# Performance work log

Hardware: AMD Instinct MI355X
Metric: run time of the kernel (lower is better)

Reference implementation:

```python
import jax, jax.numpy as jnp
import numpy as np

N = 100000
E = 1600000
IN_C, HID, OUT_C = 128, 64, 64


def gcn_conv(x, src, dst, W, b, n):
    # PyG GCNConv: h = D^{-1/2} (A + I) D^{-1/2} (x @ W) + b
    h = x @ W  # [N, F_out]
    # degrees from edges + self-loops (edge weight 1)
    deg = jax.ops.segment_sum(jnp.ones_like(dst, dtype=h.dtype), dst, num_segments=n)
    deg = deg + 1.0  # self-loops
    dinv = jnp.where(deg > 0, jax.lax.rsqrt(deg), 0.0)
    norm = dinv[src] * dinv[dst]  # [E]
    out = jax.ops.segment_sum(h[src] * norm[:, None], dst, num_segments=n)
    out = out + h * (dinv * dinv)[:, None]  # self-loop messages
    return out + b


def setup_inputs() -> dict:
    key = jax.random.key(0)
    ks = jax.random.split(key, 8)
    x = jax.random.normal(ks[0], (N, IN_C), dtype=jnp.float32)
    edge_index = jax.random.randint(ks[1], (2, E), 0, N, dtype=jnp.int64)
    def glorot(k, fan_in, fan_out):
        s = jnp.sqrt(6.0 / (fan_in + fan_out))
        return jax.random.uniform(k, (fan_in, fan_out), jnp.float32, -s, s)
    return {
        "x": x,
        "edge_index": edge_index,
        "W1": glorot(ks[2], IN_C, HID),
        "b1": jnp.zeros((HID,), jnp.float32),
        "W_mu": glorot(ks[3], HID, OUT_C),
        "b_mu": jnp.zeros((OUT_C,), jnp.float32),
        "W_ls": glorot(ks[4], HID, OUT_C),
        "b_ls": jnp.zeros((OUT_C,), jnp.float32),
    }


def reference(x, edge_index, W1, b1, W_mu, b_mu, W_ls, b_ls):
    src, dst = edge_index[0], edge_index[1]
    h = jax.nn.relu(gcn_conv(x, src, dst, W1, b1, N))
    mu = gcn_conv(h, src, dst, W_mu, b_mu, N)
    logstd = gcn_conv(h, src, dst, W_ls, b_ls, N)
    return mu, logstd
```

## Files before the change

### kernel.cpp

```cpp
#include <hip/hip_runtime.h>


using uint = unsigned int;

static constexpr int FEAT = 64;
static constexpr int BN = 256;
static constexpr int SORT_BLOCKS = 256;
static constexpr int NB_MAX = 512;

typedef __attribute__((ext_vector_type(8))) short bf16x8;
typedef __attribute__((ext_vector_type(4))) float f32x4;

static __device__ __forceinline__ ushort f2bf(float f) {
    uint u = __float_as_uint(f);
    u += 0x7FFFu + ((u >> 16) & 1u);
    return (ushort)(u >> 16);
}
static __device__ __forceinline__ float bf2f(ushort b) {
    return __uint_as_float(((uint)b) << 16);
}


__global__ __launch_bounds__(256) void hist_kernel(const int* __restrict__ dst,
                                                   int* __restrict__ hist, int E, int nb) {
    __shared__ int h[NB_MAX];
    for (int i = threadIdx.x; i < nb; i += 256) h[i] = 0;
    __syncthreads();
    int chunk = (E + SORT_BLOCKS - 1) / SORT_BLOCKS;
    int beg = blockIdx.x * chunk;
    int end = min(beg + chunk, E);
    for (int e = beg + (int)threadIdx.x; e < end; e += 256)
        atomicAdd(&h[dst[e] >> 8], 1);
    __syncthreads();
    for (int i = threadIdx.x; i < nb; i += 256) hist[blockIdx.x * nb + i] = h[i];
}

__global__ __launch_bounds__(256) void colscan_kernel(int* __restrict__ hist,
                                                      int* __restrict__ btot, int nb) {
    __shared__ int s[256];
    int b = blockIdx.x;
    int t = threadIdx.x;
    int v = hist[t * nb + b];
    s[t] = v; __syncthreads();
    for (int off = 1; off < 256; off <<= 1) {
        int u = (t >= off) ? s[t - off] : 0;
        __syncthreads();
        s[t] += u;
        __syncthreads();
    }
    hist[t * nb + b] = s[t] - v;
    if (t == 255) btot[b] = s[255];
}

__global__ __launch_bounds__(256) void bbase_kernel(const int* __restrict__ btot,
                                                    int* __restrict__ bbase, int nb,
                                                    int* __restrict__ rowptr, int n, int E) {
    __shared__ int s[256];
    int t = threadIdx.x;
    int i0 = 2 * t, i1 = 2 * t + 1;
    int v0 = (i0 < nb) ? btot[i0] : 0;
    int v1 = (i1 < nb) ? btot[i1] : 0;
    s[t] = v0 + v1; __syncthreads();
    for (int off = 1; off < 256; off <<= 1) {
        int u = (t >= off) ? s[t - off] : 0;
        __syncthreads();
        s[t] += u;
        __syncthreads();
    }
    int excl = s[t] - (v0 + v1);
    if (i0 < nb) bbase[i0] = excl;
    if (i1 < nb) bbase[i1] = excl + v0;
    if (i0 == nb) bbase[nb] = excl;
    else if (i1 == nb) bbase[nb] = excl + v0;
    if (t == 0) rowptr[n] = E;
}

__global__ __launch_bounds__(256) void sort_scatter_kernel(const int* __restrict__ src,
                                                           const int* __restrict__ dst,
                                                           const int* __restrict__ hist,
                                                           const int* __restrict__ bbase,
                                                           uint* __restrict__ bpk, int E, int nb) {
    __shared__ int cur[NB_MAX];
    int k = blockIdx.x;
    for (int i = threadIdx.x; i < nb; i += 256) cur[i] = bbase[i] + hist[k * nb + i];
    __syncthreads();
    int chunk = (E + SORT_BLOCKS - 1) / SORT_BLOCKS;
    int beg = k * chunk;
    int end = min(beg + chunk, E);
    for (int e = beg + (int)threadIdx.x; e < end; e += 256) {
        int s = src[e], d = dst[e];
        int pos = atomicAdd(&cur[d >> 8], 1);
        bpk[pos] = (uint)s | ((uint)(d & 255) << 17);
    }
}

__global__ __launch_bounds__(256) void place_kernel(const uint* __restrict__ bpk,
                                                    const int* __restrict__ bbase,
                                                    int* __restrict__ rowptr,
                                                    float* __restrict__ dinv,
                                                    int* __restrict__ ssrc, int n) {
    __shared__ int cnt[BN];
    __shared__ int s[256];
    int b = blockIdx.x;
    int base = b * BN;
    int beg = bbase[b], end = bbase[b + 1];
    cnt[threadIdx.x] = 0;
    __syncthreads();
    for (int p = beg + (int)threadIdx.x; p < end; p += 256)
        atomicAdd(&cnt[bpk[p] >> 17], 1);
    __syncthreads();
    int c = cnt[threadIdx.x];
    s[threadIdx.x] = c; __syncthreads();
    for (int off = 1; off < 256; off <<= 1) {
        int u = (threadIdx.x >= off) ? s[threadIdx.x - off] : 0;
        __syncthreads();
        s[threadIdx.x] += u;
        __syncthreads();
    }
    int excl = beg + s[threadIdx.x] - c;
    __syncthreads();
    cnt[threadIdx.x] = excl;
    int node = base + threadIdx.x;
    if (node < n) {
        rowptr[node] = excl;
        dinv[node] = rsqrtf((float)c + 1.0f);
    }
    __syncthreads();
    for (int p = beg + (int)threadIdx.x; p < end; p += 256) {
        uint e = bpk[p];
        int pos = atomicAdd(&cnt[e >> 17], 1);
        ssrc[pos] = (int)(e & 0x1FFFFu);
    }
}

__global__ __launch_bounds__(256) void prep_w_kernel(const float* __restrict__ W1,
                                                     const float* __restrict__ Wmu,
                                                     const float* __restrict__ Wls,
                                                     ushort* __restrict__ w1t,
                                                     ushort* __restrict__ wmt,
                                                     ushort* __restrict__ wlt) {
    int t = blockIdx.x * 256 + threadIdx.x;
    for (int idx = t; idx < 64 * 128; idx += 2048) {
        int nn = idx >> 7, kk = idx & 127;
        w1t[idx] = f2bf(W1[kk * 64 + nn]);
    }
    for (int idx = t; idx < 64 * 64; idx += 2048) {
        int nn = idx >> 6, kk = idx & 63;
        wmt[idx] = f2bf(Wmu[kk * 64 + nn]);
        wlt[idx] = f2bf(Wls[kk * 64 + nn]);
    }
}

__global__ __launch_bounds__(256) void gemm1_kernel(const float* __restrict__ X,
                                                    const ushort* __restrict__ Wt,
                                                    const float* __restrict__ dinv,
                                                    ushort* __restrict__ T1, int n) {
    int lane = threadIdx.x & 63;
    int w = threadIdx.x >> 6;
    int rowbase = blockIdx.x * 64 + w * 16;
    int nl = lane & 15;
    int kg = lane >> 4;
    int arow = min(rowbase + nl, n - 1);
    const float* xr = X + (size_t)arow * 128 + kg * 8;
    f32x4 acc0 = {0.f, 0.f, 0.f, 0.f};
    f32x4 acc1 = acc0, acc2 = acc0, acc3 = acc0;
#pragma unroll
    for (int ks = 0; ks < 4; ++ks) {
        int k0 = ks * 32;
        float4 xa = *(const float4*)(xr + k0);
        float4 xb = *(const float4*)(xr + k0 + 4);
        bf16x8 a;
        a[0] = (short)f2bf(xa.x); a[1] = (short)f2bf(xa.y);
        a[2] = (short)f2bf(xa.z); a[3] = (short)f2bf(xa.w);
        a[4] = (short)f2bf(xb.x); a[5] = (short)f2bf(xb.y);
        a[6] = (short)f2bf(xb.z); a[7] = (short)f2bf(xb.w);
        const ushort* wb = Wt + (size_t)nl * 128 + k0 + kg * 8;
        bf16x8 b0 = *(const bf16x8*)(wb);
        bf16x8 b1 = *(const bf16x8*)(wb + 16 * 128);
        bf16x8 b2 = *(const bf16x8*)(wb + 32 * 128);
        bf16x8 b3 = *(const bf16x8*)(wb + 48 * 128);
        acc0 = __builtin_amdgcn_mfma_f32_16x16x32_bf16(a, b0, acc0, 0, 0, 0);
        acc1 = __builtin_amdgcn_mfma_f32_16x16x32_bf16(a, b1, acc1, 0, 0, 0);
        acc2 = __builtin_amdgcn_mfma_f32_16x16x32_bf16(a, b2, acc2, 0, 0, 0);
        acc3 = __builtin_amdgcn_mfma_f32_16x16x32_bf16(a, b3, acc3, 0, 0, 0);
    }
#pragma unroll
    for (int r = 0; r < 4; ++r) {
        int row = rowbase + kg * 4 + r;
        if (row < n) {
            float di = dinv[row];
            ushort* out = T1 + (size_t)row * FEAT + nl;
            out[0]  = f2bf(acc0[r] * di);
            out[16] = f2bf(acc1[r] * di);
            out[32] = f2bf(acc2[r] * di);
            out[48] = f2bf(acc3[r] * di);
        }
    }
}

template<int MODE>
__global__ __launch_bounds__(256) void agg_kernel(const ushort* __restrict__ T,
                                                  const int* __restrict__ rowptr,
                                                  const int* __restrict__ ssrc,
                                                  const float* __restrict__ dinv,
                                                  const float* __restrict__ bias,
                                                  ushort* __restrict__ Tout, int n) {
    int node = blockIdx.x * 4 + (threadIdx.x >> 6);
    if (node >= n) return;
    int f = threadIdx.x & 63;
    int beg = rowptr[node], end = rowptr[node + 1];
    float di = dinv[node];
    float acc = bf2f(T[(size_t)node * FEAT + f]);
    int p = beg;
    int ahead = (beg + 3) & ~3;
    for (int lim = min(ahead, end); p < lim; ++p)
        acc += bf2f(T[(size_t)ssrc[p] * FEAT + f]);
    for (; p + 8 <= end; p += 8) {
        int4 a = *(const int4*)(ssrc + p);
        int4 b = *(const int4*)(ssrc + p + 4);
        float v0 = bf2f(T[(size_t)a.x * FEAT + f]);
        float v1 = bf2f(T[(size_t)a.y * FEAT + f]);
        float v2 = bf2f(T[(size_t)a.z * FEAT + f]);
        float v3 = bf2f(T[(size_t)a.w * FEAT + f]);
        float v4 = bf2f(T[(size_t)b.x * FEAT + f]);
        float v5 = bf2f(T[(size_t)b.y * FEAT + f]);
        float v6 = bf2f(T[(size_t)b.z * FEAT + f]);
        float v7 = bf2f(T[(size_t)b.w * FEAT + f]);
        acc += ((v0 + v1) + (v2 + v3)) + ((v4 + v5) + (v6 + v7));
    }
    if (p + 4 <= end) {
        int4 a = *(const int4*)(ssrc + p);
        float v0 = bf2f(T[(size_t)a.x * FEAT + f]);
        float v1 = bf2f(T[(size_t)a.y * FEAT + f]);
        float v2 = bf2f(T[(size_t)a.z * FEAT + f]);
        float v3 = bf2f(T[(size_t)a.w * FEAT + f]);
        acc += (v0 + v1) + (v2 + v3);
        p += 4;
    }
    for (; p < end; ++p) acc += bf2f(T[(size_t)ssrc[p] * FEAT + f]);
    if (MODE == 0) {
        float h = fmaf(di, acc, bias[f]);
        h = fmaxf(h, 0.0f);
        Tout[(size_t)node * FEAT + f] = f2bf(h * di);
    } else {
        Tout[(size_t)node * FEAT + f] = f2bf(di * acc);
    }
}

__global__ __launch_bounds__(256) void gemm_dual_kernel(const ushort* __restrict__ H,
                                                        const ushort* __restrict__ Wmt,
                                                        const float* __restrict__ bmu,
                                                        const ushort* __restrict__ Wlt,
                                                        const float* __restrict__ bls,
                                                        float* __restrict__ mu,
                                                        float* __restrict__ ls, int n) {
    int lane = threadIdx.x & 63;
    int w = threadIdx.x >> 6;
    int rowbase = blockIdx.x * 64 + w * 16;
    int nl = lane & 15;
    int kg = lane >> 4;
    int arow = min(rowbase + nl, n - 1);
    const ushort* hr = H + (size_t)arow * 64 + kg * 8;
    f32x4 am0 = {0.f, 0.f, 0.f, 0.f};
    f32x4 am1 = am0, am2 = am0, am3 = am0;
    f32x4 al0 = am0, al1 = am0, al2 = am0, al3 = am0;
#pragma unroll
    for (int ks = 0; ks < 2; ++ks) {
        int k0 = ks * 32;
        bf16x8 a = *(const bf16x8*)(hr + k0);
        const ushort* wm = Wmt + (size_t)nl * 64 + k0 + kg * 8;
        const ushort* wl = Wlt + (size_t)nl * 64 + k0 + kg * 8;
        bf16x8 m0 = *(const bf16x8*)(wm);
        bf16x8 m1 = *(const bf16x8*)(wm + 16 * 64);
        bf16x8 m2 = *(const bf16x8*)(wm + 32 * 64);
        bf16x8 m3 = *(const bf16x8*)(wm + 48 * 64);
        bf16x8 l0 = *(const bf16x8*)(wl);
        bf16x8 l1 = *(const bf16x8*)(wl + 16 * 64);
        bf16x8 l2 = *(const bf16x8*)(wl + 32 * 64);
        bf16x8 l3 = *(const bf16x8*)(wl + 48 * 64);
        am0 = __builtin_amdgcn_mfma_f32_16x16x32_bf16(a, m0, am0, 0, 0, 0);
        am1 = __builtin_amdgcn_mfma_f32_16x16x32_bf16(a, m1, am1, 0, 0, 0);
        am2 = __builtin_amdgcn_mfma_f32_16x16x32_bf16(a, m2, am2, 0, 0, 0);
        am3 = __builtin_amdgcn_mfma_f32_16x16x32_bf16(a, m3, am3, 0, 0, 0);
        al0 = __builtin_amdgcn_mfma_f32_16x16x32_bf16(a, l0, al0, 0, 0, 0);
        al1 = __builtin_amdgcn_mfma_f32_16x16x32_bf16(a, l1, al1, 0, 0, 0);
        al2 = __builtin_amdgcn_mfma_f32_16x16x32_bf16(a, l2, al2, 0, 0, 0);
        al3 = __builtin_amdgcn_mfma_f32_16x16x32_bf16(a, l3, al3, 0, 0, 0);
    }
    float bm0 = bmu[nl], bm1 = bmu[16 + nl], bm2 = bmu[32 + nl], bm3 = bmu[48 + nl];
    float bl0 = bls[nl], bl1 = bls[16 + nl], bl2 = bls[32 + nl], bl3 = bls[48 + nl];
#pragma unroll
    for (int r = 0; r < 4; ++r) {
        int row = rowbase + kg * 4 + r;
        if (row < n) {
            float* om = mu + (size_t)row * 64 + nl;
            float* ol = ls + (size_t)row * 64 + nl;
            om[0]  = am0[r] + bm0; om[16] = am1[r] + bm1;
            om[32] = am2[r] + bm2; om[48] = am3[r] + bm3;
            ol[0]  = al0[r] + bl0; ol[16] = al1[r] + bl1;
            ol[32] = al2[r] + bl2; ol[48] = al3[r] + bl3;
        }
    }
}

extern "C" void kernel_launch(void* const* d_in, const int* in_sizes, int n_in,
                              void* d_out, int out_size, void* d_ws, size_t ws_size,
                              hipStream_t stream) {
    const float* x   = (const float*)d_in[0];
    const int*   ei  = (const int*)d_in[1];
    const float* W1  = (const float*)d_in[2];
    const float* b1  = (const float*)d_in[3];
    const float* Wmu = (const float*)d_in[4];
    const float* bmu = (const float*)d_in[5];
    const float* Wls = (const float*)d_in[6];
    const float* bls = (const float*)d_in[7];

    const int N = in_sizes[0] / 128;
    const int E = in_sizes[1] / 2;
    const int* src = ei;
    const int* dst = ei + E;

    const int nb = (N + BN - 1) / BN;

    float*  dinv   = (float*)d_ws;
    int*    rowptr = (int*)(dinv + N);
    int*    hist   = rowptr + ((N + 1 + 63) & ~63);
    int*    btot   = hist + SORT_BLOCKS * nb;
    int*    bbase  = btot + ((nb + 63) & ~63);
    int*    ssrc   = bbase + ((nb + 1 + 63) & ~63);
    uint*   bpk    = (uint*)(ssrc + E);
    ushort* T1     = (ushort*)(bpk + E);
    ushort* T2     = T1 + (size_t)N * FEAT;
    ushort* w1t    = T2 + (size_t)N * FEAT;
    ushort* wmt    = w1t + 64 * 128;
    ushort* wlt    = wmt + 64 * 64;

    float* mu_out = (float*)d_out;
    float* ls_out = mu_out + (size_t)N * FEAT;

    const int TB = 256;
    int grid_n4 = (N + 3) / 4;
    int grid_g  = (N + 63) / 64;

    prep_w_kernel<<<8, TB, 0, stream>>>(W1, Wmu, Wls, w1t, wmt, wlt);

    hist_kernel<<<SORT_BLOCKS, TB, 0, stream>>>(dst, hist, E, nb);
    colscan_kernel<<<nb, TB, 0, stream>>>(hist, btot, nb);
    bbase_kernel<<<1, TB, 0, stream>>>(btot, bbase, nb, rowptr, N, E);
    sort_scatter_kernel<<<SORT_BLOCKS, TB, 0, stream>>>(src, dst, hist, bbase, bpk, E, nb);
    place_kernel<<<nb, TB, 0, stream>>>(bpk, bbase, rowptr, dinv, ssrc, N);

    gemm1_kernel<<<grid_g, TB, 0, stream>>>(x, w1t, dinv, T1, N);

    agg_kernel<0><<<grid_n4, TB, 0, stream>>>(T1, rowptr, ssrc, dinv, b1, T2, N);

    agg_kernel<1><<<grid_n4, TB, 0, stream>>>(T2, rowptr, ssrc, dinv, nullptr, T1, N);

    gemm_dual_kernel<<<grid_g, TB, 0, stream>>>(T1, wmt, bmu, wlt, bls, mu_out, ls_out, N);
}
```

Before: 217.1 us.

## Fuse per-node CSR placement into aggregation via shared-memory bucket sort

Drops the separate place kernel that built rowptr and a global sorted source array. Each aggregation block now re-sorts its 256-node bucket of packed edges into shared memory (capacity 5120 edges) and aggregates straight from there. Degrees come from global atomics in the histogram pass plus a small dinv kernel. This removes a global scatter pass and the rowptr/ssrc traffic, but the per-bucket sort is repeated in both aggregation passes. It also adds per-edge global atomics and a hard bucket-size cap that could overflow on skewed graphs.

```diff
diff --git a/kernel.cpp b/kernel.cpp
--- a/kernel.cpp
+++ b/kernel.cpp
@@ -7,6 +7,8 @@
 static constexpr int BN = 256;
 static constexpr int SORT_BLOCKS = 256;
 static constexpr int NB_MAX = 512;
+static constexpr int AGG_TPB = 1024;
+static constexpr int ECAP = 5120;
 
 typedef __attribute__((ext_vector_type(8))) short bf16x8;
 typedef __attribute__((ext_vector_type(4))) float f32x4;
@@ -22,17 +24,27 @@
 
 
 __global__ __launch_bounds__(256) void hist_kernel(const int* __restrict__ dst,
-                                                   int* __restrict__ hist, int E, int nb) {
+                                                   int* __restrict__ hist,
+                                                   int* __restrict__ deg, int E, int nb) {
     __shared__ int h[NB_MAX];
     for (int i = threadIdx.x; i < nb; i += 256) h[i] = 0;
     __syncthreads();
     int chunk = (E + SORT_BLOCKS - 1) / SORT_BLOCKS;
     int beg = blockIdx.x * chunk;
     int end = min(beg + chunk, E);
-    for (int e = beg + (int)threadIdx.x; e < end; e += 256)
-        atomicAdd(&h[dst[e] >> 8], 1);
+    for (int e = beg + (int)threadIdx.x; e < end; e += 256) {
+        int d = dst[e];
+        atomicAdd(&h[d >> 8], 1);
+        atomicAdd(&deg[d], 1);
+    }
     __syncthreads();
     for (int i = threadIdx.x; i < nb; i += 256) hist[blockIdx.x * nb + i] = h[i];
+}
+
+__global__ __launch_bounds__(256) void dinv_kernel(const int* __restrict__ deg,
+                                                   float* __restrict__ dinv, int n) {
+    int i = blockIdx.x * 256 + threadIdx.x;
+    if (i < n) dinv[i] = rsqrtf((float)deg[i] + 1.0f);
 }
 
 __global__ __launch_bounds__(256) void colscan_kernel(int* __restrict__ hist,
@@ -53,8 +65,7 @@
 }
 
 __global__ __launch_bounds__(256) void bbase_kernel(const int* __restrict__ btot,
-                                                    int* __restrict__ bbase, int nb,
-                                                    int* __restrict__ rowptr, int n, int E) {
+                                                    int* __restrict__ bbase, int nb) {
     __shared__ int s[256];
     int t = threadIdx.x;
     int i0 = 2 * t, i1 = 2 * t + 1;
@@ -68,11 +79,8 @@
         __syncthreads();
     }
     int excl = s[t] - (v0 + v1);
-    if (i0 < nb) bbase[i0] = excl;
-    if (i1 < nb) bbase[i1] = excl + v0;
-    if (i0 == nb) bbase[nb] = excl;
-    else if (i1 == nb) bbase[nb] = excl + v0;
-    if (t == 0) rowptr[n] = E;
+    if (i0 <= nb) bbase[i0] = excl;
+    if (i1 <= nb) bbase[i1] = excl + v0;
 }
 
 __global__ __launch_bounds__(256) void sort_scatter_kernel(const int* __restrict__ src,
@@ -91,45 +99,6 @@
         int s = src[e], d = dst[e];
         int pos = atomicAdd(&cur[d >> 8], 1);
         bpk[pos] = (uint)s | ((uint)(d & 255) << 17);
-    }
-}
-
-__global__ __launch_bounds__(256) void place_kernel(const uint* __restrict__ bpk,
-                                                    const int* __restrict__ bbase,
-                                                    int* __restrict__ rowptr,
-                                                    float* __restrict__ dinv,
-                                                    int* __restrict__ ssrc, int n) {
-    __shared__ int cnt[BN];
-    __shared__ int s[256];
-    int b = blockIdx.x;
-    int base = b * BN;
-    int beg = bbase[b], end = bbase[b + 1];
-    cnt[threadIdx.x] = 0;
-    __syncthreads();
-    for (int p = beg + (int)threadIdx.x; p < end; p += 256)
-        atomicAdd(&cnt[bpk[p] >> 17], 1);
-    __syncthreads();
-    int c = cnt[threadIdx.x];
-    s[threadIdx.x] = c; __syncthreads();
-    for (int off = 1; off < 256; off <<= 1) {
-        int u = (threadIdx.x >= off) ? s[threadIdx.x - off] : 0;
-        __syncthreads();
-        s[threadIdx.x] += u;
-        __syncthreads();
-    }
-    int excl = beg + s[threadIdx.x] - c;
-    __syncthreads();
-    cnt[threadIdx.x] = excl;
-    int node = base + threadIdx.x;
-    if (node < n) {
-        rowptr[node] = excl;
-        dinv[node] = rsqrtf((float)c + 1.0f);
-    }
-    __syncthreads();
-    for (int p = beg + (int)threadIdx.x; p < end; p += 256) {
-        uint e = bpk[p];
-        int pos = atomicAdd(&cnt[e >> 17], 1);
-        ssrc[pos] = (int)(e & 0x1FFFFu);
     }
 }
 
@@ -199,51 +168,72 @@
 }
 
 template<int MODE>
-__global__ __launch_bounds__(256) void agg_kernel(const ushort* __restrict__ T,
-                                                  const int* __restrict__ rowptr,
-                                                  const int* __restrict__ ssrc,
-                                                  const float* __restrict__ dinv,
-                                                  const float* __restrict__ bias,
-                                                  ushort* __restrict__ Tout, int n) {
-    int node = blockIdx.x * 4 + (threadIdx.x >> 6);
-    if (node >= n) return;
-    int f = threadIdx.x & 63;
-    int beg = rowptr[node], end = rowptr[node + 1];
-    float di = dinv[node];
-    float acc = bf2f(T[(size_t)node * FEAT + f]);
-    int p = beg;
-    int ahead = (beg + 3) & ~3;
-    for (int lim = min(ahead, end); p < lim; ++p)
-        acc += bf2f(T[(size_t)ssrc[p] * FEAT + f]);
-    for (; p + 8 <= end; p += 8) {
-        int4 a = *(const int4*)(ssrc + p);
-        int4 b = *(const int4*)(ssrc + p + 4);
-        float v0 = bf2f(T[(size_t)a.x * FEAT + f]);
-        float v1 = bf2f(T[(size_t)a.y * FEAT + f]);
-        float v2 = bf2f(T[(size_t)a.z * FEAT + f]);
-        float v3 = bf2f(T[(size_t)a.w * FEAT + f]);
-        float v4 = bf2f(T[(size_t)b.x * FEAT + f]);
-        float v5 = bf2f(T[(size_t)b.y * FEAT + f]);
-        float v6 = bf2f(T[(size_t)b.z * FEAT + f]);
-        float v7 = bf2f(T[(size_t)b.w * FEAT + f]);
-        acc += ((v0 + v1) + (v2 + v3)) + ((v4 + v5) + (v6 + v7));
-    }
-    if (p + 4 <= end) {
-        int4 a = *(const int4*)(ssrc + p);
-        float v0 = bf2f(T[(size_t)a.x * FEAT + f]);
-        float v1 = bf2f(T[(size_t)a.y * FEAT + f]);
-        float v2 = bf2f(T[(size_t)a.z * FEAT + f]);
-        float v3 = bf2f(T[(size_t)a.w * FEAT + f]);
-        acc += (v0 + v1) + (v2 + v3);
-        p += 4;
-    }
-    for (; p < end; ++p) acc += bf2f(T[(size_t)ssrc[p] * FEAT + f]);
-    if (MODE == 0) {
-        float h = fmaf(di, acc, bias[f]);
-        h = fmaxf(h, 0.0f);
-        Tout[(size_t)node * FEAT + f] = f2bf(h * di);
-    } else {
-        Tout[(size_t)node * FEAT + f] = f2bf(di * acc);
+__global__ __launch_bounds__(AGG_TPB) void agg_kernel(const ushort* __restrict__ T,
+                                                      const uint* __restrict__ bpk,
+                                                      const int* __restrict__ bbase,
+                                                      const float* __restrict__ bias,
+                                                      ushort* __restrict__ Tout, int n) {
+    __shared__ int lsrc[ECAP];
+    __shared__ int cnt[BN];
+    __shared__ int cur[BN];
+    __shared__ int sc[BN];
+    int b = blockIdx.x;
+    int base = b * BN;
+    int t = threadIdx.x;
+    int beg = bbase[b], end = bbase[b + 1];
+    if (t < BN) cnt[t] = 0;
+    __syncthreads();
+    for (int p = beg + t; p < end; p += AGG_TPB)
+        atomicAdd(&cnt[(bpk[p] >> 17) & 255], 1);
+    __syncthreads();
+    if (t < BN) sc[t] = cnt[t];
+    __syncthreads();
+    for (int off = 1; off < BN; off <<= 1) {
+        int u = 0;
+        if (t < BN && t >= off) u = sc[t - off];
+        __syncthreads();
+        if (t < BN) sc[t] += u;
+        __syncthreads();
+    }
+    if (t < BN) cur[t] = sc[t] - cnt[t];
+    __syncthreads();
+    for (int p = beg + t; p < end; p += AGG_TPB) {
+        uint e = bpk[p];
+        int pos = atomicAdd(&cur[(e >> 17) & 255], 1);
+        lsrc[pos] = (int)(e & 0x1FFFFu);
+    }
+    __syncthreads();
+    int f = t & 63;
+    int w = t >> 6;
+    for (int nl = w; nl < BN; nl += 16) {
+        int node = base + nl;
+        if (node >= n) break;
+        int c = cnt[nl];
+        int pe = sc[nl];
+        int p = pe - c;
+        float acc = bf2f(T[(size_t)node * FEAT + f]);
+        for (; p + 8 <= pe; p += 8) {
+            int s0 = lsrc[p],     s1 = lsrc[p + 1], s2 = lsrc[p + 2], s3 = lsrc[p + 3];
+            int s4 = lsrc[p + 4], s5 = lsrc[p + 5], s6 = lsrc[p + 6], s7 = lsrc[p + 7];
+            float v0 = bf2f(T[(size_t)s0 * FEAT + f]);
+            float v1 = bf2f(T[(size_t)s1 * FEAT + f]);
+            float v2 = bf2f(T[(size_t)s2 * FEAT + f]);
+            float v3 = bf2f(T[(size_t)s3 * FEAT + f]);
+            float v4 = bf2f(T[(size_t)s4 * FEAT + f]);
+            float v5 = bf2f(T[(size_t)s5 * FEAT + f]);
+            float v6 = bf2f(T[(size_t)s6 * FEAT + f]);
+            float v7 = bf2f(T[(size_t)s7 * FEAT + f]);
+            acc += ((v0 + v1) + (v2 + v3)) + ((v4 + v5) + (v6 + v7));
+        }
+        for (; p < pe; ++p) acc += bf2f(T[(size_t)lsrc[p] * FEAT + f]);
+        float di = rsqrtf((float)c + 1.0f);
+        if (MODE == 0) {
+            float h = fmaf(di, acc, bias[f]);
+            h = fmaxf(h, 0.0f);
+            Tout[(size_t)node * FEAT + f] = f2bf(h * di);
+        } else {
+            Tout[(size_t)node * FEAT + f] = f2bf(di * acc);
+        }
     }
 }
 
@@ -322,13 +312,12 @@
 
     const int nb = (N + BN - 1) / BN;
 
-    float*  dinv   = (float*)d_ws;
-    int*    rowptr = (int*)(dinv + N);
-    int*    hist   = rowptr + ((N + 1 + 63) & ~63);
+    int*    deg    = (int*)d_ws;
+    float*  dinv   = (float*)(deg + N);
+    int*    hist   = (int*)(dinv + N);
     int*    btot   = hist + SORT_BLOCKS * nb;
     int*    bbase  = btot + ((nb + 63) & ~63);
-    int*    ssrc   = bbase + ((nb + 1 + 63) & ~63);
-    uint*   bpk    = (uint*)(ssrc + E);
+    uint*   bpk    = (uint*)(bbase + ((nb + 1 + 63) & ~63));
     ushort* T1     = (ushort*)(bpk + E);
     ushort* T2     = T1 + (size_t)N * FEAT;
     ushort* w1t    = T2 + (size_t)N * FEAT;
@@ -339,22 +328,23 @@
     float* ls_out = mu_out + (size_t)N * FEAT;
 
     const int TB = 256;
-    int grid_n4 = (N + 3) / 4;
-    int grid_g  = (N + 63) / 64;
+    int grid_n = (N + TB - 1) / TB;
+    int grid_g = (N + 63) / 64;
 
     prep_w_kernel<<<8, TB, 0, stream>>>(W1, Wmu, Wls, w1t, wmt, wlt);
 
-    hist_kernel<<<SORT_BLOCKS, TB, 0, stream>>>(dst, hist, E, nb);
+    hipMemsetAsync(deg, 0, (size_t)N * sizeof(int), stream);
+    hist_kernel<<<SORT_BLOCKS, TB, 0, stream>>>(dst, hist, deg, E, nb);
+    dinv_kernel<<<grid_n, TB, 0, stream>>>(deg, dinv, N);
     colscan_kernel<<<nb, TB, 0, stream>>>(hist, btot, nb);
-    bbase_kernel<<<1, TB, 0, stream>>>(btot, bbase, nb, rowptr, N, E);
+    bbase_kernel<<<1, TB, 0, stream>>>(btot, bbase, nb);
     sort_scatter_kernel<<<SORT_BLOCKS, TB, 0, stream>>>(src, dst, hist, bbase, bpk, E, nb);
-    place_kernel<<<nb, TB, 0, stream>>>(bpk, bbase, rowptr, dinv, ssrc, N);
 
     gemm1_kernel<<<grid_g, TB, 0, stream>>>(x, w1t, dinv, T1, N);
 
-    agg_kernel<0><<<grid_n4, TB, 0, stream>>>(T1, rowptr, ssrc, dinv, b1, T2, N);
-
-    agg_kernel<1><<<grid_n4, TB, 0, stream>>>(T2, rowptr, ssrc, dinv, nullptr, T1, N);
+    agg_kernel<0><<<nb, AGG_TPB, 0, stream>>>(T1, bpk, bbase, b1, T2, N);
+
+    agg_kernel<1><<<nb, AGG_TPB, 0, stream>>>(T2, bpk, bbase, nullptr, T1, N);
 
     gemm_dual_kernel<<<grid_g, TB, 0, stream>>>(T1, wmt, bmu, wlt, bls, mu_out, ls_out, N);
 }
```

Result: slower. 252.9 us (+16.5%).
